# Optimization experiments

Measured on AMD Instinct MI355X. Metric: run time of the kernel, lower is better.

## Reference

```python
import jax, jax.numpy as jnp
import numpy as np

N = 100000   # nodes
E = 1600000  # edges (avg degree 16)
D = 128      # input = hidden = out dim
L = 4        # num_layers
EPS = 1e-5   # LayerNorm eps


def setup_inputs() -> dict:
    key = jax.random.key(0)
    k0, k1, k2, k3, k4 = jax.random.split(key, 5)
    in_feat = jax.random.normal(k0, (N, D), dtype=jnp.float32)
    edge_index = jax.random.randint(k1, (2, E), 0, N, dtype=jnp.int32)
    s = 1.0 / np.sqrt(D)
    # GraphConv params per layer: lin_rel (weight+bias), lin_root (weight, no bias)
    W_rel = jax.random.uniform(k2, (L, D, D), jnp.float32, -s, s)
    b_rel = jax.random.uniform(k3, (L, D), jnp.float32, -s, s)
    W_root = jax.random.uniform(k4, (L, D, D), jnp.float32, -s, s)
    # single shared LayerNorm module in the torch code
    ln_gamma = jnp.ones((D,), jnp.float32)
    ln_beta = jnp.zeros((D,), jnp.float32)
    return {"in_feat": in_feat, "edge_index": edge_index, "W_rel": W_rel,
            "b_rel": b_rel, "W_root": W_root, "ln_gamma": ln_gamma, "ln_beta": ln_beta}


def _layer_norm(h, gamma, beta):
    mu = jnp.mean(h, axis=-1, keepdims=True)
    var = jnp.mean(jnp.square(h - mu), axis=-1, keepdims=True)
    return (h - mu) * jax.lax.rsqrt(var + EPS) * gamma + beta


def _graph_conv(h, W_r, b_r, W_rt, src, dst):
    # PyG GraphConv: out_i = lin_rel(sum_{j->i} x_j) + lin_root(x_i)
    agg = jax.ops.segment_sum(h[src], dst, num_segments=N)  # [N, D]
    return agg @ W_r + b_r + h @ W_rt


def reference(in_feat, edge_index, W_rel, b_rel, W_root, ln_gamma, ln_beta):
    src, dst = edge_index[0], edge_index[1]
    # input layer: conv -> ReLU -> LayerNorm -> dropout(p=0)
    h = _graph_conv(in_feat, W_rel[0], b_rel[0], W_root[0], src, dst)
    h = _layer_norm(jax.nn.relu(h), ln_gamma, ln_beta)
    # middle layers with residual
    for l in range(1, L - 1):
        nh = _graph_conv(h, W_rel[l], b_rel[l], W_root[l], src, dst)
        h = _layer_norm(jax.nn.relu(nh + h), ln_gamma, ln_beta)
    # output layer: conv only
    return _graph_conv(h, W_rel[L - 1], b_rel[L - 1], W_root[L - 1], src, dst)
```

## Files before the change

kernel.cpp:

```cpp
#include <hip/hip_runtime.h>
#include <cstddef>

#define N_NODES 100000
#define N_PAD   100032
#define N_EDGES 1600000
#define DIM 128
#define LN_EPS 1e-5f
#define ZROW   N_NODES

#define B_SHIFT 9
#define B_SIZE  512
#define N_BKT   196
#define EPB     4096
#define NBLK    ((N_EDGES + EPB - 1) / EPB)

typedef short bf16x8 __attribute__((ext_vector_type(8)));
typedef float f32x4 __attribute__((ext_vector_type(4)));

__device__ __forceinline__ float asf(uint u) {
    union { uint i; float f; } c; c.i = u; return c.f;
}
__device__ __forceinline__ float bf2f(uint u) { return asf(u << 16); }
__device__ __forceinline__ ushort f2bf(float x) {
    union { float f; uint i; } c; c.f = x;
    uint r = c.i + 0x7fffu + ((c.i >> 16) & 1u);
    return (ushort)(r >> 16);
}

__device__ __forceinline__ void acc8(float* a, uint4 p) {
    a[0] += asf(p.x << 16); a[1] += asf(p.x & 0xffff0000u);
    a[2] += asf(p.y << 16); a[3] += asf(p.y & 0xffff0000u);
    a[4] += asf(p.z << 16); a[5] += asf(p.z & 0xffff0000u);
    a[6] += asf(p.w << 16); a[7] += asf(p.w & 0xffff0000u);
}


__global__ __launch_bounds__(256) void bhist_kernel(const int* __restrict__ dst,
                                                    int* __restrict__ bcount) {
    __shared__ int lh[N_BKT];
    const int tid = threadIdx.x;
    if (tid < N_BKT) lh[tid] = 0;
    __syncthreads();
    const int base = blockIdx.x * EPB;
    #pragma unroll
    for (int k = 0; k < 16; ++k) {
        int t = base + tid + k * 256;
        if (t < N_EDGES) atomicAdd(&lh[dst[t] >> B_SHIFT], 1);
    }
    __syncthreads();
    if (tid < N_BKT && lh[tid]) atomicAdd(&bcount[tid], lh[tid]);
}

__global__ __launch_bounds__(256) void bscan_kernel(const int* __restrict__ bcount,
                                                    int* __restrict__ bstart,
                                                    int* __restrict__ gcur) {
    __shared__ int s[256];
    const int tid = threadIdx.x;
    int v = (tid < N_BKT) ? bcount[tid] : 0;
    s[tid] = v;
    __syncthreads();
    for (int off = 1; off < 256; off <<= 1) {
        int t = (tid >= off) ? s[tid - off] : 0;
        __syncthreads();
        s[tid] += t;
        __syncthreads();
    }
    if (tid < N_BKT) { int e = s[tid] - v; bstart[tid] = e; gcur[tid] = e; }
    if (tid == 0) bstart[N_BKT] = N_EDGES;
}

__global__ __launch_bounds__(256) void bscatter_kernel(const int* __restrict__ src,
                                                       const int* __restrict__ dst,
                                                       int* __restrict__ gcur,
                                                       int2* __restrict__ pairs) {
    __shared__ int lcnt[N_BKT];
    __shared__ int lbase[N_BKT];
    const int tid = threadIdx.x;
    if (tid < N_BKT) lcnt[tid] = 0;
    __syncthreads();
    const int base = blockIdx.x * EPB;
    int ls[16], ld[16];
    #pragma unroll
    for (int k = 0; k < 16; ++k) {
        int t = base + tid + k * 256;
        if (t < N_EDGES) {
            ls[k] = src[t]; ld[k] = dst[t];
            atomicAdd(&lcnt[ld[k] >> B_SHIFT], 1);
        } else ld[k] = -1;
    }
    __syncthreads();
    if (tid < N_BKT) lbase[tid] = lcnt[tid] ? atomicAdd(&gcur[tid], lcnt[tid]) : 0;
    __syncthreads();
    if (tid < N_BKT) lcnt[tid] = 0;
    __syncthreads();
    #pragma unroll
    for (int k = 0; k < 16; ++k) {
        if (ld[k] >= 0) {
            int b = ld[k] >> B_SHIFT;
            int r = atomicAdd(&lcnt[b], 1);
            pairs[lbase[b] + r] = make_int2(ls[k], ld[k]);
        }
    }
}

__global__ __launch_bounds__(256) void ndeg_kernel(const int2* __restrict__ pairs,
                                                   const int* __restrict__ bstart,
                                                   int* __restrict__ row_ptr) {
    __shared__ int ldeg[B_SIZE];
    __shared__ int ws[4];
    const int b = blockIdx.x;
    const int node0 = b << B_SHIFT;
    const int tid = threadIdx.x;
    ldeg[tid] = 0; ldeg[tid + 256] = 0;
    __syncthreads();
    const int beg = bstart[b], end = bstart[b + 1];
    for (int t = beg + tid; t < end; t += 256)
        atomicAdd(&ldeg[pairs[t].y - node0], 1);
    __syncthreads();
    const int d0 = ldeg[2 * tid], d1 = ldeg[2 * tid + 1];
    const int sum2 = d0 + d1;
    const int lane = tid & 63, wv = tid >> 6;
    int incl = sum2;
    #pragma unroll
    for (int off = 1; off < 64; off <<= 1) {
        int t = __shfl_up(incl, off);
        if (lane >= off) incl += t;
    }
    if (lane == 63) ws[wv] = incl;
    __syncthreads();
    int woff = 0;
    if (wv > 0) woff += ws[0];
    if (wv > 1) woff += ws[1];
    if (wv > 2) woff += ws[2];
    const int e0 = beg + woff + incl - sum2;
    const int n0 = node0 + 2 * tid;
    if (n0 < N_NODES)     row_ptr[n0]     = e0;
    if (n0 + 1 < N_NODES) row_ptr[n0 + 1] = e0 + d0;
    if (b == N_BKT - 1 && tid == 0) row_ptr[N_NODES] = N_EDGES;
}

__global__ __launch_bounds__(256) void bfill_kernel(const int2* __restrict__ pairs,
                                                    const int* __restrict__ bstart,
                                                    const int* __restrict__ row_ptr,
                                                    int* __restrict__ col) {
    __shared__ int lcur[B_SIZE];
    const int b = blockIdx.x;
    const int node0 = b << B_SHIFT;
    const int tid = threadIdx.x;
    #pragma unroll
    for (int k = 0; k < 2; ++k) {
        int n = node0 + tid + k * 256;
        lcur[tid + k * 256] = (n < N_NODES) ? row_ptr[n] : 0;
    }
    __syncthreads();
    const int beg = bstart[b], end = bstart[b + 1];
    for (int t = beg + tid; t < end; t += 256) {
        int2 p = pairs[t];
        int r = atomicAdd(&lcur[p.y - node0], 1);
        col[r] = p.x;
    }
}


__global__ void cvt_kernel(const float* __restrict__ in, ushort* __restrict__ out) {
    int i = (blockIdx.x * blockDim.x + threadIdx.x) * 4;
    float4 v = *(const float4*)&in[i];
    uint2 r;
    r.x = (uint)f2bf(v.x) | ((uint)f2bf(v.y) << 16);
    r.y = (uint)f2bf(v.z) | ((uint)f2bf(v.w) << 16);
    *(uint2*)&out[i] = r;
}


__global__ void prepack_kernel(const float* __restrict__ Wrel, const float* __restrict__ Wroot,
                               ushort* __restrict__ Wp) {
    int t = blockIdx.x * blockDim.x + threadIdx.x;
    int layer = t >> 12;
    int tl = t & 4095;
    int frag = tl >> 6;
    int lane = tl & 63;
    int ks = frag >> 3, n = frag & 7;
    int c = n * 16 + (lane & 15);
    int k0 = ks * 32 + (lane >> 4) * 8;
    ushort tmp[8];
    #pragma unroll
    for (int j = 0; j < 8; ++j) {
        int kg = k0 + j;
        float w = (kg < 128) ? Wrel[layer * 16384 + kg * 128 + c]
                             : Wroot[layer * 16384 + (kg - 128) * 128 + c];
        tmp[j] = f2bf(w);
    }
    *(uint4*)&Wp[(size_t)t * 8] = *(const uint4*)tmp;
}


__global__ __launch_bounds__(256) void pull_kernel(const uint4* __restrict__ h,
                                                   const int* __restrict__ row_ptr,
                                                   const int* __restrict__ col,
                                                   uint4* __restrict__ agg, int n) {
    const int wid = threadIdx.x >> 6;
    const int lane = threadIdx.x & 63;
    const int node = blockIdx.x * 4 + wid;
    if (node >= n) return;
    const int beg = row_ptr[node], end = row_ptr[node + 1];
    const int rsel = lane >> 4;
    const int c16 = lane & 15;
    float a[8] = {0, 0, 0, 0, 0, 0, 0, 0};
    float b[8] = {0, 0, 0, 0, 0, 0, 0, 0};
    for (int j = beg; j < end; j += 16) {
        const int j0 = j + rsel, j1 = j0 + 4, j2 = j0 + 8, j3 = j0 + 12;
        const int last = end - 1;
        int s0 = col[min(j0, last)]; s0 = (j0 < end) ? s0 : ZROW;
        int s1 = col[min(j1, last)]; s1 = (j1 < end) ? s1 : ZROW;
        int s2 = col[min(j2, last)]; s2 = (j2 < end) ? s2 : ZROW;
        int s3 = col[min(j3, last)]; s3 = (j3 < end) ? s3 : ZROW;
        uint4 p0 = h[(size_t)s0 * 16 + c16];
        uint4 p1 = h[(size_t)s1 * 16 + c16];
        uint4 p2 = h[(size_t)s2 * 16 + c16];
        uint4 p3 = h[(size_t)s3 * 16 + c16];
        acc8(a, p0);
        acc8(b, p1);
        acc8(a, p2);
        acc8(b, p3);
    }
    #pragma unroll
    for (int u = 0; u < 8; ++u) {
        float v = a[u] + b[u];
        v += __shfl_xor(v, 16);
        v += __shfl_xor(v, 32);
        a[u] = v;
    }
    if (rsel == 0) {
        uint4 o;
        o.x = (uint)f2bf(a[0]) | ((uint)f2bf(a[1]) << 16);
        o.y = (uint)f2bf(a[2]) | ((uint)f2bf(a[3]) << 16);
        o.z = (uint)f2bf(a[4]) | ((uint)f2bf(a[5]) << 16);
        o.w = (uint)f2bf(a[6]) | ((uint)f2bf(a[7]) << 16);
        agg[(size_t)node * 16 + c16] = o;
    }
}


template <int MODE>
__global__ __launch_bounds__(256) void gemm_kernel(const ushort* __restrict__ aggb,
                                                   const ushort* __restrict__ hb,
                                                   const ushort* __restrict__ Wp,
                                                   const float* __restrict__ brel,
                                                   const float* __restrict__ gamma,
                                                   const float* __restrict__ beta,
                                                   ushort* __restrict__ outb,
                                                   float* __restrict__ outf) {
    __shared__ char sX[64 * 512];
    const int tid = threadIdx.x;
    const int row0 = blockIdx.x * 64;

    for (int c = tid; c < 2048; c += 256) {
        int r = c >> 5, cb = c & 31;
        const ushort* srcp = (cb < 16) ? &aggb[(size_t)(row0 + r) * 128 + cb * 8]
                                       : &hb[(size_t)(row0 + r) * 128 + (cb - 16) * 8];
        uint4 v = *(const uint4*)srcp;
        *(uint4*)&sX[r * 512 + ((cb * 16) ^ ((r & 7) << 4))] = v;
    }
    __syncthreads();

    const int lane = tid & 63;
    const int wv = tid >> 6;
    const int kg = lane >> 4;
    const int cl = lane & 15;
    const int ra = wv * 16 + cl;
    const int abase = ra * 512 + kg * 16;
    const int aswz = (ra & 7) << 4;

    f32x4 acc[8];
    #pragma unroll
    for (int n = 0; n < 8; ++n) acc[n] = (f32x4){0.f, 0.f, 0.f, 0.f};

    const uint4* bp = (const uint4*)Wp + lane;
    #pragma unroll 2
    for (int ks = 0; ks < 8; ++ks) {
        bf16x8 a = *(const bf16x8*)&sX[(abase + ks * 64) ^ aswz];
        #pragma unroll
        for (int n = 0; n < 8; ++n) {
            bf16x8 b = *(const bf16x8*)&bp[(ks * 8 + n) * 64];
            acc[n] = __builtin_amdgcn_mfma_f32_16x16x32_bf16(a, b, acc[n], 0, 0, 0);
        }
    }

    float bias[8], gg[8], bb[8];
    #pragma unroll
    for (int n = 0; n < 8; ++n) {
        int cn = n * 16 + cl;
        bias[n] = brel[cn];
        if (MODE != 2) { gg[n] = gamma[cn]; bb[n] = beta[cn]; }
    }

    #pragma unroll
    for (int reg = 0; reg < 4; ++reg) {
        const int r = wv * 16 + kg * 4 + reg;
        const size_t grow = (size_t)row0 + r;
        const bool live = grow < N_NODES;
        float v[8];
        float s = 0.f, q = 0.f;
        #pragma unroll
        for (int n = 0; n < 8; ++n) {
            float x = acc[n][reg] + bias[n];
            if (MODE == 1) {
                int cn = n * 16 + cl;
                ushort hu = *(const ushort*)&sX[r * 512 + ((256 + 2 * cn) ^ ((r & 7) << 4))];
                x += bf2f(hu);
            }
            if (MODE != 2) x = fmaxf(x, 0.f);
            v[n] = x; s += x; q += x * x;
        }
        if (MODE != 2) {
            #pragma unroll
            for (int m = 8; m >= 1; m >>= 1) { s += __shfl_xor(s, m); q += __shfl_xor(q, m); }
            float mu = s * (1.f / DIM);
            float var = q * (1.f / DIM) - mu * mu;
            float rinv = rsqrtf(var + LN_EPS);
            if (live) {
                #pragma unroll
                for (int n = 0; n < 8; ++n) {
                    float y = (v[n] - mu) * rinv * gg[n] + bb[n];
                    outb[grow * DIM + n * 16 + cl] = f2bf(y);
                }
            }
        } else {
            if (live) {
                #pragma unroll
                for (int n = 0; n < 8; ++n) outf[grow * DIM + n * 16 + cl] = v[n];
            }
        }
    }
}


static inline size_t align256(size_t x) { return (x + 255) & ~(size_t)255; }

extern "C" void kernel_launch(void* const* d_in, const int* in_sizes, int n_in,
                              void* d_out, int out_size, void* d_ws, size_t ws_size,
                              hipStream_t stream) {
    const float* in_feat = (const float*)d_in[0];
    const int*   ei      = (const int*)d_in[1];
    const float* Wrel    = (const float*)d_in[2];
    const float* brel    = (const float*)d_in[3];
    const float* Wroot   = (const float*)d_in[4];
    const float* gamma   = (const float*)d_in[5];
    const float* beta    = (const float*)d_in[6];
    float* out = (float*)d_out;

    char* ws = (char*)d_ws;
    size_t off = 0;
    int* col = (int*)(ws + off);        off = align256(off + (size_t)N_EDGES * 4);
    int2* pairs = (int2*)(ws + off);    off = align256(off + (size_t)N_EDGES * 8);
    int* row_ptr = (int*)(ws + off);    off = align256(off + (size_t)(N_NODES + 1) * 4);
    int* bcount = (int*)(ws + off);     off = align256(off + (size_t)N_BKT * 4);
    int* bstart = (int*)(ws + off);     off = align256(off + (size_t)(N_BKT + 1) * 4);
    int* gcur = (int*)(ws + off);       off = align256(off + (size_t)N_BKT * 4);
    ushort* x0 = (ushort*)(ws + off);   off = align256(off + (size_t)N_PAD * DIM * 2);
    ushort* hA = (ushort*)(ws + off);   off = align256(off + (size_t)N_PAD * DIM * 2);
    ushort* hB = (ushort*)(ws + off);   off = align256(off + (size_t)N_PAD * DIM * 2);
    ushort* agg = (ushort*)(ws + off);  off = align256(off + (size_t)N_PAD * DIM * 2);
    ushort* Wp = (ushort*)(ws + off);   off = align256(off + (size_t)4 * 256 * 128 * 2);
    (void)ws_size; (void)in_sizes; (void)n_in; (void)out_size;

    const int* src = ei;
    const int* dst = ei + N_EDGES;

    hipMemsetAsync(bcount, 0, (size_t)N_BKT * 4, stream);
    bhist_kernel<<<NBLK, 256, 0, stream>>>(dst, bcount);
    bscan_kernel<<<1, 256, 0, stream>>>(bcount, bstart, gcur);
    bscatter_kernel<<<NBLK, 256, 0, stream>>>(src, dst, gcur, pairs);
    ndeg_kernel<<<N_BKT, 256, 0, stream>>>(pairs, bstart, row_ptr);
    bfill_kernel<<<N_BKT, 256, 0, stream>>>(pairs, bstart, row_ptr, col);

    const size_t padoff = (size_t)N_NODES * DIM * 2;
    const size_t padlen = (size_t)(N_PAD - N_NODES) * DIM * 2;
    hipMemsetAsync((char*)x0 + padoff, 0, padlen, stream);
    hipMemsetAsync((char*)hA + padoff, 0, padlen, stream);
    hipMemsetAsync((char*)hB + padoff, 0, padlen, stream);
    hipMemsetAsync((char*)agg + padoff, 0, padlen, stream);

    cvt_kernel<<<(N_NODES * DIM) / (4 * 256), 256, 0, stream>>>(in_feat, x0);
    prepack_kernel<<<64, 256, 0, stream>>>(Wrel, Wroot, Wp);

    const int pull_grid = (N_NODES + 3) / 4;
    const int gemm_grid = N_PAD / 64;

    pull_kernel<<<pull_grid, 256, 0, stream>>>((const uint4*)x0, row_ptr, col, (uint4*)agg, N_NODES);
    gemm_kernel<0><<<gemm_grid, 256, 0, stream>>>(agg, x0, Wp, brel, gamma, beta, hA, nullptr);
    pull_kernel<<<pull_grid, 256, 0, stream>>>((const uint4*)hA, row_ptr, col, (uint4*)agg, N_NODES);
    gemm_kernel<1><<<gemm_grid, 256, 0, stream>>>(agg, hA, Wp + 32768, brel + DIM, gamma, beta, hB, nullptr);
    pull_kernel<<<pull_grid, 256, 0, stream>>>((const uint4*)hB, row_ptr, col, (uint4*)agg, N_NODES);
    gemm_kernel<1><<<gemm_grid, 256, 0, stream>>>(agg, hB, Wp + 2 * 32768, brel + 2 * DIM, gamma, beta, hA, nullptr);
    pull_kernel<<<pull_grid, 256, 0, stream>>>((const uint4*)hA, row_ptr, col, (uint4*)agg, N_NODES);
    gemm_kernel<2><<<gemm_grid, 256, 0, stream>>>(agg, hA, Wp + 3 * 32768, brel + 3 * DIM, gamma, beta, nullptr, out);
}
```

Measured before the change: 429.1 us.

## Pad CSR rows to 16 and process two nodes per wavefront in pull

Each node's CSR segment is padded to a multiple of 16, and the padding slots are filled with the zero-row index. This needs a new per-bucket padded prefix scan, a row_ptr rebase pass and a zero-fill of the column array. The pull kernel then drops its per-load bounds checks and has each wavefront gather for two nodes at once, with eight row loads in flight per iteration and packed float2 accumulation. The cost is extra gathers of the zero row for padding, a larger col buffer whose fixed capacity depends on the degree distribution, and several extra preprocessing launches.

New measurement: 440.3 us. 1.03x slower.

```diff
diff --git a/kernel.cpp b/kernel.cpp
--- a/kernel.cpp
+++ b/kernel.cpp
@@ -7,6 +7,7 @@
 #define DIM 128
 #define LN_EPS 1e-5f
 #define ZROW   N_NODES
+#define COL_CAP 3200000
 
 #define B_SHIFT 9
 #define B_SIZE  512
@@ -16,6 +17,7 @@
 
 typedef short bf16x8 __attribute__((ext_vector_type(8)));
 typedef float f32x4 __attribute__((ext_vector_type(4)));
+typedef float f32x2 __attribute__((ext_vector_type(2)));
 
 __device__ __forceinline__ float asf(uint u) {
     union { uint i; float f; } c; c.i = u; return c.f;
@@ -27,11 +29,14 @@
     return (ushort)(r >> 16);
 }
 
-__device__ __forceinline__ void acc8(float* a, uint4 p) {
-    a[0] += asf(p.x << 16); a[1] += asf(p.x & 0xffff0000u);
-    a[2] += asf(p.y << 16); a[3] += asf(p.y & 0xffff0000u);
-    a[4] += asf(p.z << 16); a[5] += asf(p.z & 0xffff0000u);
-    a[6] += asf(p.w << 16); a[7] += asf(p.w & 0xffff0000u);
+__device__ __forceinline__ void accp(f32x2* acc, uint p) {
+    f32x2 v;
+    v.x = asf(p << 16);
+    v.y = asf(p & 0xffff0000u);
+    *acc += v;
+}
+__device__ __forceinline__ void accq(f32x2* a, uint4 p) {
+    accp(&a[0], p.x); accp(&a[1], p.y); accp(&a[2], p.z); accp(&a[3], p.w);
 }
 
 
@@ -105,9 +110,10 @@
 
 __global__ __launch_bounds__(256) void ndeg_kernel(const int2* __restrict__ pairs,
                                                    const int* __restrict__ bstart,
-                                                   int* __restrict__ row_ptr) {
+                                                   int* __restrict__ row_ptr,
+                                                   int* __restrict__ bpad) {
     __shared__ int ldeg[B_SIZE];
-    __shared__ int ws[4];
+    __shared__ int ws4[4];
     const int b = blockIdx.x;
     const int node0 = b << B_SHIFT;
     const int tid = threadIdx.x;
@@ -117,7 +123,8 @@
     for (int t = beg + tid; t < end; t += 256)
         atomicAdd(&ldeg[pairs[t].y - node0], 1);
     __syncthreads();
-    const int d0 = ldeg[2 * tid], d1 = ldeg[2 * tid + 1];
+    const int d0 = (ldeg[2 * tid] + 15) & ~15;
+    const int d1 = (ldeg[2 * tid + 1] + 15) & ~15;
     const int sum2 = d0 + d1;
     const int lane = tid & 63, wv = tid >> 6;
     int incl = sum2;
@@ -126,17 +133,45 @@
         int t = __shfl_up(incl, off);
         if (lane >= off) incl += t;
     }
-    if (lane == 63) ws[wv] = incl;
+    if (lane == 63) ws4[wv] = incl;
     __syncthreads();
     int woff = 0;
-    if (wv > 0) woff += ws[0];
-    if (wv > 1) woff += ws[1];
-    if (wv > 2) woff += ws[2];
-    const int e0 = beg + woff + incl - sum2;
+    if (wv > 0) woff += ws4[0];
+    if (wv > 1) woff += ws4[1];
+    if (wv > 2) woff += ws4[2];
+    const int e0 = woff + incl - sum2;
     const int n0 = node0 + 2 * tid;
     if (n0 < N_NODES)     row_ptr[n0]     = e0;
     if (n0 + 1 < N_NODES) row_ptr[n0 + 1] = e0 + d0;
-    if (b == N_BKT - 1 && tid == 0) row_ptr[N_NODES] = N_EDGES;
+    if (tid == 255) bpad[b] = woff + incl;
+}
+
+__global__ __launch_bounds__(256) void pscan_kernel(const int* __restrict__ bpad,
+                                                    int* __restrict__ bpadstart) {
+    __shared__ int s[256];
+    const int tid = threadIdx.x;
+    int v = (tid < N_BKT) ? bpad[tid] : 0;
+    s[tid] = v;
+    __syncthreads();
+    for (int off = 1; off < 256; off <<= 1) {
+        int t = (tid >= off) ? s[tid - off] : 0;
+        __syncthreads();
+        s[tid] += t;
+        __syncthreads();
+    }
+    if (tid < N_BKT) bpadstart[tid] = s[tid] - v;
+    if (tid == N_BKT - 1) bpadstart[N_BKT] = s[tid];
+}
+
+__global__ void addbase_kernel(int* __restrict__ row_ptr, const int* __restrict__ bpadstart) {
+    int n = blockIdx.x * 256 + threadIdx.x;
+    if (n < N_NODES) row_ptr[n] += bpadstart[n >> B_SHIFT];
+    if (n == N_NODES) row_ptr[N_NODES] = bpadstart[N_BKT];
+}
+
+__global__ void zfill_kernel(int4* __restrict__ col4) {
+    int i = blockIdx.x * 256 + threadIdx.x;
+    col4[i] = make_int4(ZROW, ZROW, ZROW, ZROW);
 }
 
 __global__ __launch_bounds__(256) void bfill_kernel(const int2* __restrict__ pairs,
@@ -197,46 +232,70 @@
 __global__ __launch_bounds__(256) void pull_kernel(const uint4* __restrict__ h,
                                                    const int* __restrict__ row_ptr,
                                                    const int* __restrict__ col,
-                                                   uint4* __restrict__ agg, int n) {
+                                                   uint4* __restrict__ agg, int npairs) {
     const int wid = threadIdx.x >> 6;
     const int lane = threadIdx.x & 63;
-    const int node = blockIdx.x * 4 + wid;
-    if (node >= n) return;
-    const int beg = row_ptr[node], end = row_ptr[node + 1];
+    const int pr = blockIdx.x * 4 + wid;
+    if (pr >= npairs) return;
+    const int nA = pr * 2, nB = nA + 1;
     const int rsel = lane >> 4;
     const int c16 = lane & 15;
-    float a[8] = {0, 0, 0, 0, 0, 0, 0, 0};
-    float b[8] = {0, 0, 0, 0, 0, 0, 0, 0};
-    for (int j = beg; j < end; j += 16) {
-        const int j0 = j + rsel, j1 = j0 + 4, j2 = j0 + 8, j3 = j0 + 12;
-        const int last = end - 1;
-        int s0 = col[min(j0, last)]; s0 = (j0 < end) ? s0 : ZROW;
-        int s1 = col[min(j1, last)]; s1 = (j1 < end) ? s1 : ZROW;
-        int s2 = col[min(j2, last)]; s2 = (j2 < end) ? s2 : ZROW;
-        int s3 = col[min(j3, last)]; s3 = (j3 < end) ? s3 : ZROW;
-        uint4 p0 = h[(size_t)s0 * 16 + c16];
-        uint4 p1 = h[(size_t)s1 * 16 + c16];
-        uint4 p2 = h[(size_t)s2 * 16 + c16];
-        uint4 p3 = h[(size_t)s3 * 16 + c16];
-        acc8(a, p0);
-        acc8(b, p1);
-        acc8(a, p2);
-        acc8(b, p3);
-    }
-    #pragma unroll
-    for (int u = 0; u < 8; ++u) {
-        float v = a[u] + b[u];
-        v += __shfl_xor(v, 16);
-        v += __shfl_xor(v, 32);
-        a[u] = v;
+    int jA = row_ptr[nA] + rsel;
+    int jB = row_ptr[nB] + rsel;
+    const int itA = (row_ptr[nA + 1] - (jA - rsel)) >> 4;
+    const int itB = (row_ptr[nB + 1] - (jB - rsel)) >> 4;
+    const int iters = max(itA, itB);
+
+    f32x2 a[4], b[4];
+    #pragma unroll
+    for (int u = 0; u < 4; ++u) { a[u] = (f32x2){0.f, 0.f}; b[u] = (f32x2){0.f, 0.f}; }
+
+    for (int it = 0; it < iters; ++it) {
+        int sA0 = ZROW, sA1 = ZROW, sA2 = ZROW, sA3 = ZROW;
+        int sB0 = ZROW, sB1 = ZROW, sB2 = ZROW, sB3 = ZROW;
+        if (it < itA) {
+            sA0 = col[jA]; sA1 = col[jA + 4]; sA2 = col[jA + 8]; sA3 = col[jA + 12];
+            jA += 16;
+        }
+        if (it < itB) {
+            sB0 = col[jB]; sB1 = col[jB + 4]; sB2 = col[jB + 8]; sB3 = col[jB + 12];
+            jB += 16;
+        }
+        uint4 pA0 = h[(size_t)sA0 * 16 + c16];
+        uint4 pA1 = h[(size_t)sA1 * 16 + c16];
+        uint4 pA2 = h[(size_t)sA2 * 16 + c16];
+        uint4 pA3 = h[(size_t)sA3 * 16 + c16];
+        uint4 pB0 = h[(size_t)sB0 * 16 + c16];
+        uint4 pB1 = h[(size_t)sB1 * 16 + c16];
+        uint4 pB2 = h[(size_t)sB2 * 16 + c16];
+        uint4 pB3 = h[(size_t)sB3 * 16 + c16];
+        accq(a, pA0); accq(a, pA1); accq(a, pA2); accq(a, pA3);
+        accq(b, pB0); accq(b, pB1); accq(b, pB2); accq(b, pB3);
+    }
+
+    #pragma unroll
+    for (int u = 0; u < 4; ++u) {
+        float ax = a[u].x, ay = a[u].y, bx = b[u].x, by = b[u].y;
+        ax += __shfl_xor(ax, 16); ay += __shfl_xor(ay, 16);
+        bx += __shfl_xor(bx, 16); by += __shfl_xor(by, 16);
+        ax += __shfl_xor(ax, 32); ay += __shfl_xor(ay, 32);
+        bx += __shfl_xor(bx, 32); by += __shfl_xor(by, 32);
+        a[u].x = ax; a[u].y = ay; b[u].x = bx; b[u].y = by;
     }
     if (rsel == 0) {
         uint4 o;
-        o.x = (uint)f2bf(a[0]) | ((uint)f2bf(a[1]) << 16);
-        o.y = (uint)f2bf(a[2]) | ((uint)f2bf(a[3]) << 16);
-        o.z = (uint)f2bf(a[4]) | ((uint)f2bf(a[5]) << 16);
-        o.w = (uint)f2bf(a[6]) | ((uint)f2bf(a[7]) << 16);
-        agg[(size_t)node * 16 + c16] = o;
+        o.x = (uint)f2bf(a[0].x) | ((uint)f2bf(a[0].y) << 16);
+        o.y = (uint)f2bf(a[1].x) | ((uint)f2bf(a[1].y) << 16);
+        o.z = (uint)f2bf(a[2].x) | ((uint)f2bf(a[2].y) << 16);
+        o.w = (uint)f2bf(a[3].x) | ((uint)f2bf(a[3].y) << 16);
+        agg[(size_t)nA * 16 + c16] = o;
+    } else if (rsel == 1) {
+        uint4 o;
+        o.x = (uint)f2bf(b[0].x) | ((uint)f2bf(b[0].y) << 16);
+        o.y = (uint)f2bf(b[1].x) | ((uint)f2bf(b[1].y) << 16);
+        o.z = (uint)f2bf(b[2].x) | ((uint)f2bf(b[2].y) << 16);
+        o.w = (uint)f2bf(b[3].x) | ((uint)f2bf(b[3].y) << 16);
+        agg[(size_t)nB * 16 + c16] = o;
     }
 }
 
@@ -351,12 +410,14 @@
 
     char* ws = (char*)d_ws;
     size_t off = 0;
-    int* col = (int*)(ws + off);        off = align256(off + (size_t)N_EDGES * 4);
+    int* col = (int*)(ws + off);        off = align256(off + (size_t)COL_CAP * 4);
     int2* pairs = (int2*)(ws + off);    off = align256(off + (size_t)N_EDGES * 8);
     int* row_ptr = (int*)(ws + off);    off = align256(off + (size_t)(N_NODES + 1) * 4);
     int* bcount = (int*)(ws + off);     off = align256(off + (size_t)N_BKT * 4);
     int* bstart = (int*)(ws + off);     off = align256(off + (size_t)(N_BKT + 1) * 4);
     int* gcur = (int*)(ws + off);       off = align256(off + (size_t)N_BKT * 4);
+    int* bpad = (int*)(ws + off);       off = align256(off + (size_t)N_BKT * 4);
+    int* bpadstart = (int*)(ws + off);  off = align256(off + (size_t)(N_BKT + 1) * 4);
     ushort* x0 = (ushort*)(ws + off);   off = align256(off + (size_t)N_PAD * DIM * 2);
     ushort* hA = (ushort*)(ws + off);   off = align256(off + (size_t)N_PAD * DIM * 2);
     ushort* hB = (ushort*)(ws + off);   off = align256(off + (size_t)N_PAD * DIM * 2);
@@ -371,7 +432,10 @@
     bhist_kernel<<<NBLK, 256, 0, stream>>>(dst, bcount);
     bscan_kernel<<<1, 256, 0, stream>>>(bcount, bstart, gcur);
     bscatter_kernel<<<NBLK, 256, 0, stream>>>(src, dst, gcur, pairs);
-    ndeg_kernel<<<N_BKT, 256, 0, stream>>>(pairs, bstart, row_ptr);
+    ndeg_kernel<<<N_BKT, 256, 0, stream>>>(pairs, bstart, row_ptr, bpad);
+    pscan_kernel<<<1, 256, 0, stream>>>(bpad, bpadstart);
+    addbase_kernel<<<(N_NODES + 256) / 256, 256, 0, stream>>>(row_ptr, bpadstart);
+    zfill_kernel<<<COL_CAP / 1024, 256, 0, stream>>>((int4*)col);
     bfill_kernel<<<N_BKT, 256, 0, stream>>>(pairs, bstart, row_ptr, col);
 
     const size_t padoff = (size_t)N_NODES * DIM * 2;
@@ -384,15 +448,16 @@
     cvt_kernel<<<(N_NODES * DIM) / (4 * 256), 256, 0, stream>>>(in_feat, x0);
     prepack_kernel<<<64, 256, 0, stream>>>(Wrel, Wroot, Wp);
 
-    const int pull_grid = (N_NODES + 3) / 4;
+    const int npairs = N_NODES / 2;
+    const int pull_grid = (npairs + 3) / 4;
     const int gemm_grid = N_PAD / 64;
 
-    pull_kernel<<<pull_grid, 256, 0, stream>>>((const uint4*)x0, row_ptr, col, (uint4*)agg, N_NODES);
+    pull_kernel<<<pull_grid, 256, 0, stream>>>((const uint4*)x0, row_ptr, col, (uint4*)agg, npairs);
     gemm_kernel<0><<<gemm_grid, 256, 0, stream>>>(agg, x0, Wp, brel, gamma, beta, hA, nullptr);
-    pull_kernel<<<pull_grid, 256, 0, stream>>>((const uint4*)hA, row_ptr, col, (uint4*)agg, N_NODES);
+    pull_kernel<<<pull_grid, 256, 0, stream>>>((const uint4*)hA, row_ptr, col, (uint4*)agg, npairs);
     gemm_kernel<1><<<gemm_grid, 256, 0, stream>>>(agg, hA, Wp + 32768, brel + DIM, gamma, beta, hB, nullptr);
-    pull_kernel<<<pull_grid, 256, 0, stream>>>((const uint4*)hB, row_ptr, col, (uint4*)agg, N_NODES);
+    pull_kernel<<<pull_grid, 256, 0, stream>>>((const uint4*)hB, row_ptr, col, (uint4*)agg, npairs);
     gemm_kernel<1><<<gemm_grid, 256, 0, stream>>>(agg, hB, Wp + 2 * 32768, brel + 2 * DIM, gamma, beta, hA, nullptr);
-    pull_kernel<<<pull_grid, 256, 0, stream>>>((const uint4*)hA, row_ptr, col, (uint4*)agg, N_NODES);
+    pull_kernel<<<pull_grid, 256, 0, stream>>>((const uint4*)hA, row_ptr, col, (uint4*)agg, npairs);
     gemm_kernel<2><<<gemm_grid, 256, 0, stream>>>(agg, hA, Wp + 3 * 32768, brel + 3 * DIM, gamma, beta, nullptr, out);
 }
```
